# Kernel optimization log

Measured on AMD Instinct MI355X. Metric: run time of the kernel, lower is better.

## Reference

```python
import jax, jax.numpy as jnp
import numpy as np

B, H, L = 8, 256, 8192

def setup_inputs() -> dict:
    key = jax.random.key(0)
    k1, k2, k3 = jax.random.split(key, 3)
    u = jax.random.normal(k1, (B, H, L), dtype=jnp.float32)
    K = jax.random.normal(k2, (H, L), dtype=jnp.float32)
    # D ~ uniform_ring with min=max=1.0, field='real' -> random signs on unit ring
    D = jnp.where(jax.random.uniform(k3, (H,)) < 0.5, -1.0, 1.0).astype(jnp.float32)
    return {"u": u, "K": K, "D": D}

def reference(u, K, D):
    # FFT-based circular long convolution per channel: y = ifft(fft(u) * fft(K)).real
    u_s = jnp.fft.fft(u, axis=-1)            # (B,H,L) complex
    k_s = jnp.fft.fft(K, axis=-1)            # (H,L)   complex
    y = jnp.fft.ifft(u_s * k_s[None], axis=-1).real  # (B,H,L)
    y = y + D[None, :, None] * u             # skip connection D*u
    y = jnp.tanh(y)
    return y
```

## Files before the change

kernel.cpp:

```cpp
#include <hip/hip_runtime.h>
#include <math.h>


#define LL 8192
#define NT 512
#define HH 256
#define TWO_PI 6.2831853071795864f
#define CP8  0.92387953251129f
#define SP8  0.38268343236509f
#define CP4  0.70710678118654752f
#define SP4  0.70710678118654752f

__device__ __forceinline__ int SW(int e) {
    return e ^ ((e >> 3) & 0x18) ^ ((e >> 6) & 7);
}
__device__ __forceinline__ float fast_tanh(float x) {
    float e = __expf(2.0f * x);
    return 1.0f - 2.0f / (e + 1.0f);
}

template<int JT>
__device__ __forceinline__ void fill_pyr_cs(float c0, float s0, float Er, float Ei,
                                            float* twr, float* twi) {
    const int off = (1 << JT) - 1;
    twr[off] = c0; twi[off] = s0;
    #pragma unroll
    for (int m = 1; m < (1 << JT); ++m) {
        const float pr = twr[off + m - 1], pi = twi[off + m - 1];
        twr[off + m] = pr * Er - pi * Ei;
        twi[off + m] = pr * Ei + pi * Er;
    }
    #pragma unroll
    for (int j = JT - 1; j >= 0; --j) {
        #pragma unroll
        for (int m = 0; m < (1 << j); ++m) {
            const float a = twr[(2 << j) - 1 + m], b = twi[(2 << j) - 1 + m];
            twr[(1 << j) - 1 + m] = a * a - b * b;
            twi[(1 << j) - 1 + m] = 2.0f * a * b;
        }
    }
}
template<int JT>
__device__ __forceinline__ void fill_pyr(float ang0, float Er, float Ei,
                                         float* twr, float* twi) {
    float s, c;
    __sincosf(ang0, &s, &c);
    fill_pyr_cs<JT>(c, s, Er, Ei, twr, twi);
}

template<int R2>
__device__ __forceinline__ void dif_apply(float* xr, float* xi,
                                          const float* twr, const float* twi) {
    #pragma unroll
    for (int j = R2 - 1; j >= 0; --j) {
        #pragma unroll
        for (int q = 0; q < (1 << (R2 - 1)); ++q) {
            const int mm = q & ((1 << j) - 1);
            const int m0 = ((q >> j) << (j + 1)) | mm;
            const int m1 = m0 + (1 << j);
            const float wr = twr[(1 << j) - 1 + mm], wi = twi[(1 << j) - 1 + mm];
            const float ar = xr[m0], ai = xi[m0], br = xr[m1], bi = xi[m1];
            xr[m0] = ar + br; xi[m0] = ai + bi;
            const float dr = ar - br, di = ai - bi;
            xr[m1] = dr * wr - di * wi;
            xi[m1] = dr * wi + di * wr;
        }
    }
}
template<int R2>
__device__ __forceinline__ void dit_apply(float* xr, float* xi,
                                          const float* twr, const float* twi) {
    #pragma unroll
    for (int j = 0; j < R2; ++j) {
        #pragma unroll
        for (int q = 0; q < (1 << (R2 - 1)); ++q) {
            const int mm = q & ((1 << j) - 1);
            const int m0 = ((q >> j) << (j + 1)) | mm;
            const int m1 = m0 + (1 << j);
            const float wr = twr[(1 << j) - 1 + mm], wi = twi[(1 << j) - 1 + mm];
            const float br = xr[m1] * wr - xi[m1] * wi;
            const float bi = xr[m1] * wi + xi[m1] * wr;
            const float ar = xr[m0], ai = xi[m0];
            xr[m0] = ar + br; xi[m0] = ai + bi;
            xr[m1] = ar - br; xi[m1] = ai - bi;
        }
    }
}

__device__ __forceinline__ void fwd_A(float* xr, float* xi, int tid,
                                      float* re, float* im) {
    float twr[15], twi[15];
    fill_pyr<3>(-(TWO_PI / 8192.0f) * (float)tid, CP8, -SP8, twr, twi);
    dif_apply<4>(xr, xi, twr, twi);
    #pragma unroll
    for (int m = 0; m < 16; ++m) {
        const int p = SW(tid + (m << 9));
        re[p] = xr[m]; im[p] = xi[m];
    }
}

template<bool INV>
__device__ __forceinline__ void mid_M1(float* re, float* im, int lane, int wv) {
    float twr[7], twi[7];
    const float sgn = INV ? 1.0f : -1.0f;
    fill_pyr<2>(sgn * (TWO_PI / 512.0f) * (float)lane, CP4, sgn * SP4, twr, twi);
    #pragma unroll
    for (int r = 0; r < 2; ++r) {
        const int base = (((wv << 1) | r) << 9) + lane;
        float ar[8], ai[8];
        #pragma unroll
        for (int j = 0; j < 8; ++j) {
            const int p = SW(base + (j << 6));
            ar[j] = re[p]; ai[j] = im[p];
        }
        if (INV) dit_apply<3>(ar, ai, twr, twi);
        else     dif_apply<3>(ar, ai, twr, twi);
        #pragma unroll
        for (int j = 0; j < 8; ++j) {
            const int p = SW(base + (j << 6));
            re[p] = ar[j]; im[p] = ai[j];
        }
    }
}

template<bool INV>
__device__ __forceinline__ void mid_M2(float* re, float* im, int lane, int wv) {
    float twr[7], twi[7];
    const float sgn = INV ? 1.0f : -1.0f;
    fill_pyr<2>(sgn * (TWO_PI / 64.0f) * (float)(lane & 7), CP4, sgn * SP4, twr, twi);
    const int sub = ((lane >> 3) << 6) + (lane & 7);
    #pragma unroll
    for (int r = 0; r < 2; ++r) {
        const int base = (((wv << 1) | r) << 9) + sub;
        float ar[8], ai[8];
        #pragma unroll
        for (int j = 0; j < 8; ++j) {
            const int p = SW(base + (j << 3));
            ar[j] = re[p]; ai[j] = im[p];
        }
        if (INV) dit_apply<3>(ar, ai, twr, twi);
        else     dif_apply<3>(ar, ai, twr, twi);
        #pragma unroll
        for (int j = 0; j < 8; ++j) {
            const int p = SW(base + (j << 3));
            re[p] = ar[j]; im[p] = ai[j];
        }
    }
}

__global__ __launch_bounds__(NT, 4) void kfft_kernel(const float* __restrict__ K,
                                                     const float* __restrict__ D,
                                                     float2* __restrict__ Kf) {
    __shared__ float re[LL];
    __shared__ float im[LL];
    const int h = blockIdx.x;
    const int tid = threadIdx.x;
    const float* Kr = K + (size_t)h * LL;
    float xr[16], xi[16];
    #pragma unroll
    for (int m = 0; m < 16; ++m) {
        xr[m] = Kr[tid + (m << 9)];
        xi[m] = 0.0f;
    }
    fwd_A(xr, xi, tid, re, im);
    __syncthreads();

    const int lane = tid & 63, wv = tid >> 6;
    mid_M1<false>(re, im, lane, wv);
    mid_M2<false>(re, im, lane, wv);

    {
        const float dh = D[h];
        const float invN = 1.0f / (float)LL;
        float twd_r[7], twd_i[7];
        fill_pyr_cs<2>(1.0f, 0.0f, CP4, -SP4, twd_r, twd_i);
        #pragma unroll
        for (int r = 0; r < 2; ++r) {
            const int eb = (((wv << 1) | r) << 9) + (lane << 3);
            float yr[8], yi[8];
            #pragma unroll
            for (int j = 0; j < 8; ++j) {
                const int p = SW(eb + j);
                yr[j] = re[p]; yi[j] = im[p];
            }
            dif_apply<3>(yr, yi, twd_r, twd_i);
            float4* o4 = (float4*)(Kf + (size_t)h * LL + eb);
            #pragma unroll
            for (int jj = 0; jj < 4; ++jj) {
                float4 v;
                v.x = (yr[2 * jj]     + dh) * invN; v.y = yi[2 * jj]     * invN;
                v.z = (yr[2 * jj + 1] + dh) * invN; v.w = yi[2 * jj + 1] * invN;
                o4[jj] = v;
            }
        }
    }
}

__global__ __launch_bounds__(NT, 4) void conv_kernel(const float* __restrict__ u,
                                                     const float2* __restrict__ Kf,
                                                     float* __restrict__ out) {
    __shared__ float re[LL];
    __shared__ float im[LL];
    const int tid = threadIdx.x;
    const int h = blockIdx.x & (HH - 1);
    const int pr_ = blockIdx.x >> 8;
    const size_t off0 = ((size_t)(pr_ * 2) * HH + h) * LL;
    const size_t off1 = off0 + (size_t)HH * LL;
    const float* u0 = u + off0;
    const float* u1 = u + off1;

    float xr[16], xi[16];
    #pragma unroll
    for (int m = 0; m < 16; ++m) {
        xr[m] = u0[tid + (m << 9)];
        xi[m] = u1[tid + (m << 9)];
    }
    fwd_A(xr, xi, tid, re, im);
    __syncthreads();

    const int lane = tid & 63, wv = tid >> 6;
    const float2* kf = Kf + (size_t)h * LL;

    float kwr[2][8], kwi[2][8];
    #pragma unroll
    for (int r = 0; r < 2; ++r) {
        const int eb = (((wv << 1) | r) << 9) + (lane << 3);
        const float4* kp = (const float4*)(kf + eb);
        #pragma unroll
        for (int jj = 0; jj < 4; ++jj) {
            const float4 v = kp[jj];
            kwr[r][2 * jj] = v.x;     kwi[r][2 * jj] = v.y;
            kwr[r][2 * jj + 1] = v.z; kwi[r][2 * jj + 1] = v.w;
        }
    }

    mid_M1<false>(re, im, lane, wv);
    mid_M2<false>(re, im, lane, wv);

    {
        float twd_r[7], twd_i[7], twu_r[7], twu_i[7];
        fill_pyr_cs<2>(1.0f, 0.0f, CP4, -SP4, twd_r, twd_i);
        fill_pyr_cs<2>(1.0f, 0.0f, CP4, SP4, twu_r, twu_i);
        #pragma unroll
        for (int r = 0; r < 2; ++r) {
            const int eb = (((wv << 1) | r) << 9) + (lane << 3);
            float yr[8], yi[8];
            #pragma unroll
            for (int j = 0; j < 8; ++j) {
                const int p = SW(eb + j);
                yr[j] = re[p]; yi[j] = im[p];
            }
            dif_apply<3>(yr, yi, twd_r, twd_i);
            #pragma unroll
            for (int j = 0; j < 8; ++j) {
                const float a = yr[j], b = yi[j];
                yr[j] = a * kwr[r][j] - b * kwi[r][j];
                yi[j] = a * kwi[r][j] + b * kwr[r][j];
            }
            dit_apply<3>(yr, yi, twu_r, twu_i);
            #pragma unroll
            for (int j = 0; j < 8; ++j) {
                const int p = SW(eb + j);
                re[p] = yr[j]; im[p] = yi[j];
            }
        }
    }

    mid_M2<true>(re, im, lane, wv);
    mid_M1<true>(re, im, lane, wv);
    __syncthreads();

    {
        float twr[15], twi[15];
        #pragma unroll
        for (int m = 0; m < 16; ++m) {
            const int p = SW(tid + (m << 9));
            xr[m] = re[p]; xi[m] = im[p];
        }
        fill_pyr<3>((TWO_PI / 8192.0f) * (float)tid, CP8, SP8, twr, twi);
        dit_apply<4>(xr, xi, twr, twi);
    }
    float* o0 = out + off0;
    float* o1 = out + off1;
    #pragma unroll
    for (int m = 0; m < 16; ++m) {
        const int n = tid + (m << 9);
        o0[n] = fast_tanh(xr[m]);
        o1[n] = fast_tanh(xi[m]);
    }
}

extern "C" void kernel_launch(void* const* d_in, const int* in_sizes, int n_in,
                              void* d_out, int out_size, void* d_ws, size_t ws_size,
                              hipStream_t stream) {
    const float* u = (const float*)d_in[0];
    const float* K = (const float*)d_in[1];
    const float* D = (const float*)d_in[2];
    float* out = (float*)d_out;
    float2* Kf = (float2*)d_ws;

    kfft_kernel<<<dim3(HH), dim3(NT), 0, stream>>>(K, D, Kf);
    conv_kernel<<<dim3(4 * HH), dim3(NT), 0, stream>>>(u, Kf, out);
}
```

Before: 150.5 us.

## Restructure FFT to 1024 threads with 8-point radix stages and shuffle final butterfly

```diff
diff --git a/kernel.cpp b/kernel.cpp
--- a/kernel.cpp
+++ b/kernel.cpp
@@ -3,7 +3,7 @@
 
 
 #define LL 8192
-#define NT 512
+#define NT 1024
 #define HH 256
 #define TWO_PI 6.2831853071795864f
 #define CP8  0.92387953251129f
@@ -12,7 +12,7 @@
 #define SP4  0.70710678118654752f
 
 __device__ __forceinline__ int SW(int e) {
-    return e ^ ((e >> 3) & 0x18) ^ ((e >> 6) & 7);
+    return e ^ ((e >> 3) & 0x10) ^ ((e >> 5) & 0x0E);
 }
 __device__ __forceinline__ float fast_tanh(float x) {
     float e = __expf(2.0f * x);
@@ -86,69 +86,92 @@
         }
     }
 }
+template<int R2>
+__device__ __forceinline__ void dit_apply_c(float* xr, float* xi,
+                                            const float* twr, const float* twi) {
+    #pragma unroll
+    for (int j = 0; j < R2; ++j) {
+        #pragma unroll
+        for (int q = 0; q < (1 << (R2 - 1)); ++q) {
+            const int mm = q & ((1 << j) - 1);
+            const int m0 = ((q >> j) << (j + 1)) | mm;
+            const int m1 = m0 + (1 << j);
+            const float wr = twr[(1 << j) - 1 + mm], wi = -twi[(1 << j) - 1 + mm];
+            const float br = xr[m1] * wr - xi[m1] * wi;
+            const float bi = xr[m1] * wi + xi[m1] * wr;
+            const float ar = xr[m0], ai = xi[m0];
+            xr[m0] = ar + br; xi[m0] = ai + bi;
+            xr[m1] = ar - br; xi[m1] = ai - bi;
+        }
+    }
+}
+
+__device__ __forceinline__ void bfly1_shfl(float* yr, float* yi, float s) {
+    #pragma unroll
+    for (int j = 0; j < 8; ++j) {
+        const float vr = __shfl_xor(yr[j], 1);
+        const float vi = __shfl_xor(yi[j], 1);
+        yr[j] = fmaf(yr[j], s, vr);
+        yi[j] = fmaf(yi[j], s, vi);
+    }
+}
 
 __device__ __forceinline__ void fwd_A(float* xr, float* xi, int tid,
                                       float* re, float* im) {
-    float twr[15], twi[15];
-    fill_pyr<3>(-(TWO_PI / 8192.0f) * (float)tid, CP8, -SP8, twr, twi);
-    dif_apply<4>(xr, xi, twr, twi);
-    #pragma unroll
-    for (int m = 0; m < 16; ++m) {
-        const int p = SW(tid + (m << 9));
+    float twr[7], twi[7];
+    fill_pyr<2>(-(TWO_PI / 8192.0f) * (float)tid, CP4, -SP4, twr, twi);
+    dif_apply<3>(xr, xi, twr, twi);
+    #pragma unroll
+    for (int m = 0; m < 8; ++m) {
+        const int p = SW(tid + (m << 10));
         re[p] = xr[m]; im[p] = xi[m];
     }
 }
 
 template<bool INV>
-__device__ __forceinline__ void mid_M1(float* re, float* im, int lane, int wv) {
+__device__ __forceinline__ void mid_M1(float* re, float* im, int t7, int cb) {
     float twr[7], twi[7];
     const float sgn = INV ? 1.0f : -1.0f;
-    fill_pyr<2>(sgn * (TWO_PI / 512.0f) * (float)lane, CP4, sgn * SP4, twr, twi);
-    #pragma unroll
-    for (int r = 0; r < 2; ++r) {
-        const int base = (((wv << 1) | r) << 9) + lane;
-        float ar[8], ai[8];
-        #pragma unroll
-        for (int j = 0; j < 8; ++j) {
-            const int p = SW(base + (j << 6));
-            ar[j] = re[p]; ai[j] = im[p];
-        }
-        if (INV) dit_apply<3>(ar, ai, twr, twi);
-        else     dif_apply<3>(ar, ai, twr, twi);
-        #pragma unroll
-        for (int j = 0; j < 8; ++j) {
-            const int p = SW(base + (j << 6));
-            re[p] = ar[j]; im[p] = ai[j];
-        }
+    fill_pyr<2>(sgn * (TWO_PI / 1024.0f) * (float)t7, CP4, sgn * SP4, twr, twi);
+    const int base = cb + t7;
+    float ar[8], ai[8];
+    #pragma unroll
+    for (int j = 0; j < 8; ++j) {
+        const int p = SW(base + (j << 7));
+        ar[j] = re[p]; ai[j] = im[p];
+    }
+    if (INV) dit_apply<3>(ar, ai, twr, twi);
+    else     dif_apply<3>(ar, ai, twr, twi);
+    #pragma unroll
+    for (int j = 0; j < 8; ++j) {
+        const int p = SW(base + (j << 7));
+        re[p] = ar[j]; im[p] = ai[j];
     }
 }
 
 template<bool INV>
-__device__ __forceinline__ void mid_M2(float* re, float* im, int lane, int wv) {
+__device__ __forceinline__ void mid_M2(float* re, float* im, int t7, int cb) {
     float twr[7], twi[7];
     const float sgn = INV ? 1.0f : -1.0f;
-    fill_pyr<2>(sgn * (TWO_PI / 64.0f) * (float)(lane & 7), CP4, sgn * SP4, twr, twi);
-    const int sub = ((lane >> 3) << 6) + (lane & 7);
-    #pragma unroll
-    for (int r = 0; r < 2; ++r) {
-        const int base = (((wv << 1) | r) << 9) + sub;
-        float ar[8], ai[8];
-        #pragma unroll
-        for (int j = 0; j < 8; ++j) {
-            const int p = SW(base + (j << 3));
-            ar[j] = re[p]; ai[j] = im[p];
-        }
-        if (INV) dit_apply<3>(ar, ai, twr, twi);
-        else     dif_apply<3>(ar, ai, twr, twi);
-        #pragma unroll
-        for (int j = 0; j < 8; ++j) {
-            const int p = SW(base + (j << 3));
-            re[p] = ar[j]; im[p] = ai[j];
-        }
-    }
-}
-
-__global__ __launch_bounds__(NT, 4) void kfft_kernel(const float* __restrict__ K,
+    const int r_ = t7 & 15;
+    fill_pyr<2>(sgn * (TWO_PI / 128.0f) * (float)r_, CP4, sgn * SP4, twr, twi);
+    const int base = cb + ((t7 >> 4) << 7) + r_;
+    float ar[8], ai[8];
+    #pragma unroll
+    for (int j = 0; j < 8; ++j) {
+        const int p = SW(base + (j << 4));
+        ar[j] = re[p]; ai[j] = im[p];
+    }
+    if (INV) dit_apply<3>(ar, ai, twr, twi);
+    else     dif_apply<3>(ar, ai, twr, twi);
+    #pragma unroll
+    for (int j = 0; j < 8; ++j) {
+        const int p = SW(base + (j << 4));
+        re[p] = ar[j]; im[p] = ai[j];
+    }
+}
+
+__global__ __launch_bounds__(NT, 8) void kfft_kernel(const float* __restrict__ K,
                                                      const float* __restrict__ D,
                                                      float2* __restrict__ Kf) {
     __shared__ float re[LL];
@@ -156,47 +179,49 @@
     const int h = blockIdx.x;
     const int tid = threadIdx.x;
     const float* Kr = K + (size_t)h * LL;
-    float xr[16], xi[16];
-    #pragma unroll
-    for (int m = 0; m < 16; ++m) {
-        xr[m] = Kr[tid + (m << 9)];
+    float xr[8], xi[8];
+    #pragma unroll
+    for (int m = 0; m < 8; ++m) {
+        xr[m] = Kr[tid + (m << 10)];
         xi[m] = 0.0f;
     }
     fwd_A(xr, xi, tid, re, im);
     __syncthreads();
 
-    const int lane = tid & 63, wv = tid >> 6;
-    mid_M1<false>(re, im, lane, wv);
-    mid_M2<false>(re, im, lane, wv);
+    const int t7 = tid & 127;
+    const int cb = (tid >> 7) << 10;
+    mid_M1<false>(re, im, t7, cb);
+    __syncthreads();
+    mid_M2<false>(re, im, t7, cb);
 
     {
+        const int g_ = t7 >> 1, par = t7 & 1;
         const float dh = D[h];
         const float invN = 1.0f / (float)LL;
-        float twd_r[7], twd_i[7];
-        fill_pyr_cs<2>(1.0f, 0.0f, CP4, -SP4, twd_r, twd_i);
-        #pragma unroll
-        for (int r = 0; r < 2; ++r) {
-            const int eb = (((wv << 1) | r) << 9) + (lane << 3);
-            float yr[8], yi[8];
-            #pragma unroll
-            for (int j = 0; j < 8; ++j) {
-                const int p = SW(eb + j);
-                yr[j] = re[p]; yi[j] = im[p];
-            }
-            dif_apply<3>(yr, yi, twd_r, twd_i);
-            float4* o4 = (float4*)(Kf + (size_t)h * LL + eb);
-            #pragma unroll
-            for (int jj = 0; jj < 4; ++jj) {
-                float4 v;
-                v.x = (yr[2 * jj]     + dh) * invN; v.y = yi[2 * jj]     * invN;
-                v.z = (yr[2 * jj + 1] + dh) * invN; v.w = yi[2 * jj + 1] * invN;
-                o4[jj] = v;
-            }
-        }
-    }
-}
-
-__global__ __launch_bounds__(NT, 4) void conv_kernel(const float* __restrict__ u,
+        float twr[7], twi[7];
+        fill_pyr_cs<2>(par ? CP8 : 1.0f, par ? -SP8 : 0.0f, CP4, -SP4, twr, twi);
+        const int base = cb + (g_ << 4) + par;
+        const float s = par ? -1.0f : 1.0f;
+        float yr[8], yi[8];
+        #pragma unroll
+        for (int j = 0; j < 8; ++j) {
+            const int p = SW(base + (j << 1));
+            yr[j] = re[p]; yi[j] = im[p];
+        }
+        dif_apply<3>(yr, yi, twr, twi);
+        bfly1_shfl(yr, yi, s);
+        float4* o4 = (float4*)(Kf + (size_t)h * LL + cb + (t7 << 3));
+        #pragma unroll
+        for (int jj = 0; jj < 4; ++jj) {
+            float4 v;
+            v.x = (yr[2 * jj]     + dh) * invN; v.y = yi[2 * jj]     * invN;
+            v.z = (yr[2 * jj + 1] + dh) * invN; v.w = yi[2 * jj + 1] * invN;
+            o4[jj] = v;
+        }
+    }
+}
+
+__global__ __launch_bounds__(NT, 8) void conv_kernel(const float* __restrict__ u,
                                                      const float2* __restrict__ Kf,
                                                      float* __restrict__ out) {
     __shared__ float re[LL];
@@ -209,82 +234,82 @@
     const float* u0 = u + off0;
     const float* u1 = u + off1;
 
-    float xr[16], xi[16];
-    #pragma unroll
-    for (int m = 0; m < 16; ++m) {
-        xr[m] = u0[tid + (m << 9)];
-        xi[m] = u1[tid + (m << 9)];
+    float xr[8], xi[8];
+    #pragma unroll
+    for (int m = 0; m < 8; ++m) {
+        xr[m] = u0[tid + (m << 10)];
+        xi[m] = u1[tid + (m << 10)];
     }
     fwd_A(xr, xi, tid, re, im);
     __syncthreads();
 
-    const int lane = tid & 63, wv = tid >> 6;
-    const float2* kf = Kf + (size_t)h * LL;
-
-    float kwr[2][8], kwi[2][8];
-    #pragma unroll
-    for (int r = 0; r < 2; ++r) {
-        const int eb = (((wv << 1) | r) << 9) + (lane << 3);
-        const float4* kp = (const float4*)(kf + eb);
+    const int t7 = tid & 127;
+    const int cb = (tid >> 7) << 10;
+
+    float kwr[8], kwi[8];
+    {
+        const float4* kp = (const float4*)(Kf + (size_t)h * LL + cb + (t7 << 3));
         #pragma unroll
         for (int jj = 0; jj < 4; ++jj) {
             const float4 v = kp[jj];
-            kwr[r][2 * jj] = v.x;     kwi[r][2 * jj] = v.y;
-            kwr[r][2 * jj + 1] = v.z; kwi[r][2 * jj + 1] = v.w;
-        }
-    }
-
-    mid_M1<false>(re, im, lane, wv);
-    mid_M2<false>(re, im, lane, wv);
+            kwr[2 * jj]     = v.x; kwi[2 * jj]     = v.y;
+            kwr[2 * jj + 1] = v.z; kwi[2 * jj + 1] = v.w;
+        }
+    }
+
+    mid_M1<false>(re, im, t7, cb);
+    __syncthreads();
+    mid_M2<false>(re, im, t7, cb);
 
     {
-        float twd_r[7], twd_i[7], twu_r[7], twu_i[7];
-        fill_pyr_cs<2>(1.0f, 0.0f, CP4, -SP4, twd_r, twd_i);
-        fill_pyr_cs<2>(1.0f, 0.0f, CP4, SP4, twu_r, twu_i);
-        #pragma unroll
-        for (int r = 0; r < 2; ++r) {
-            const int eb = (((wv << 1) | r) << 9) + (lane << 3);
-            float yr[8], yi[8];
-            #pragma unroll
-            for (int j = 0; j < 8; ++j) {
-                const int p = SW(eb + j);
-                yr[j] = re[p]; yi[j] = im[p];
-            }
-            dif_apply<3>(yr, yi, twd_r, twd_i);
-            #pragma unroll
-            for (int j = 0; j < 8; ++j) {
-                const float a = yr[j], b = yi[j];
-                yr[j] = a * kwr[r][j] - b * kwi[r][j];
-                yi[j] = a * kwi[r][j] + b * kwr[r][j];
-            }
-            dit_apply<3>(yr, yi, twu_r, twu_i);
-            #pragma unroll
-            for (int j = 0; j < 8; ++j) {
-                const int p = SW(eb + j);
-                re[p] = yr[j]; im[p] = yi[j];
-            }
-        }
-    }
-
-    mid_M2<true>(re, im, lane, wv);
-    mid_M1<true>(re, im, lane, wv);
+        const int g_ = t7 >> 1, par = t7 & 1;
+        float twr[7], twi[7];
+        fill_pyr_cs<2>(par ? CP8 : 1.0f, par ? -SP8 : 0.0f, CP4, -SP4, twr, twi);
+        const int base = cb + (g_ << 4) + par;
+        const float s = par ? -1.0f : 1.0f;
+        float yr[8], yi[8];
+        #pragma unroll
+        for (int j = 0; j < 8; ++j) {
+            const int p = SW(base + (j << 1));
+            yr[j] = re[p]; yi[j] = im[p];
+        }
+        dif_apply<3>(yr, yi, twr, twi);
+        bfly1_shfl(yr, yi, s);
+        #pragma unroll
+        for (int j = 0; j < 8; ++j) {
+            const float a = yr[j], bb = yi[j];
+            yr[j] = a * kwr[j] - bb * kwi[j];
+            yi[j] = a * kwi[j] + bb * kwr[j];
+        }
+        bfly1_shfl(yr, yi, s);
+        dit_apply_c<3>(yr, yi, twr, twi);
+        #pragma unroll
+        for (int j = 0; j < 8; ++j) {
+            const int p = SW(base + (j << 1));
+            re[p] = yr[j]; im[p] = yi[j];
+        }
+    }
+
+    mid_M2<true>(re, im, t7, cb);
+    __syncthreads();
+    mid_M1<true>(re, im, t7, cb);
     __syncthreads();
 
     {
-        float twr[15], twi[15];
-        #pragma unroll
-        for (int m = 0; m < 16; ++m) {
-            const int p = SW(tid + (m << 9));
+        float twr[7], twi[7];
+        #pragma unroll
+        for (int m = 0; m < 8; ++m) {
+            const int p = SW(tid + (m << 10));
             xr[m] = re[p]; xi[m] = im[p];
         }
-        fill_pyr<3>((TWO_PI / 8192.0f) * (float)tid, CP8, SP8, twr, twi);
-        dit_apply<4>(xr, xi, twr, twi);
+        fill_pyr<2>((TWO_PI / 8192.0f) * (float)tid, CP4, SP4, twr, twi);
+        dit_apply<3>(xr, xi, twr, twi);
     }
     float* o0 = out + off0;
     float* o1 = out + off1;
     #pragma unroll
-    for (int m = 0; m < 16; ++m) {
-        const int n = tid + (m << 9);
+    for (int m = 0; m < 8; ++m) {
+        const int n = tid + (m << 10);
         o0[n] = fast_tanh(xr[m]);
         o1[n] = fast_tanh(xi[m]);
     }
```

Measured after the change: 189.1 us. +25.6%, slower.

## Split kernel FFT into radix-4 pass plus smaller sub-FFT kernel; retune LDS swizzle

Applied to the files above, without the earlier changes.

```diff
diff --git a/kernel.cpp b/kernel.cpp
--- a/kernel.cpp
+++ b/kernel.cpp
@@ -12,7 +12,10 @@
 #define SP4  0.70710678118654752f
 
 __device__ __forceinline__ int SW(int e) {
-    return e ^ ((e >> 3) & 0x18) ^ ((e >> 6) & 7);
+    return e ^ ((e >> 3) & 0x18) ^ ((e >> 5) & 0x0E);
+}
+__device__ __forceinline__ int SW2(int e) {
+    return e ^ (((e >> 5) & 7) << 2);
 }
 __device__ __forceinline__ float fast_tanh(float x) {
     float e = __expf(2.0f * x);
@@ -87,6 +90,7 @@
     }
 }
 
+
 __device__ __forceinline__ void fwd_A(float* xr, float* xi, int tid,
                                       float* re, float* im) {
     float twr[15], twi[15];
@@ -144,54 +148,6 @@
         for (int j = 0; j < 8; ++j) {
             const int p = SW(base + (j << 3));
             re[p] = ar[j]; im[p] = ai[j];
-        }
-    }
-}
-
-__global__ __launch_bounds__(NT, 4) void kfft_kernel(const float* __restrict__ K,
-                                                     const float* __restrict__ D,
-                                                     float2* __restrict__ Kf) {
-    __shared__ float re[LL];
-    __shared__ float im[LL];
-    const int h = blockIdx.x;
-    const int tid = threadIdx.x;
-    const float* Kr = K + (size_t)h * LL;
-    float xr[16], xi[16];
-    #pragma unroll
-    for (int m = 0; m < 16; ++m) {
-        xr[m] = Kr[tid + (m << 9)];
-        xi[m] = 0.0f;
-    }
-    fwd_A(xr, xi, tid, re, im);
-    __syncthreads();
-
-    const int lane = tid & 63, wv = tid >> 6;
-    mid_M1<false>(re, im, lane, wv);
-    mid_M2<false>(re, im, lane, wv);
-
-    {
-        const float dh = D[h];
-        const float invN = 1.0f / (float)LL;
-        float twd_r[7], twd_i[7];
-        fill_pyr_cs<2>(1.0f, 0.0f, CP4, -SP4, twd_r, twd_i);
-        #pragma unroll
-        for (int r = 0; r < 2; ++r) {
-            const int eb = (((wv << 1) | r) << 9) + (lane << 3);
-            float yr[8], yi[8];
-            #pragma unroll
-            for (int j = 0; j < 8; ++j) {
-                const int p = SW(eb + j);
-                yr[j] = re[p]; yi[j] = im[p];
-            }
-            dif_apply<3>(yr, yi, twd_r, twd_i);
-            float4* o4 = (float4*)(Kf + (size_t)h * LL + eb);
-            #pragma unroll
-            for (int jj = 0; jj < 4; ++jj) {
-                float4 v;
-                v.x = (yr[2 * jj]     + dh) * invN; v.y = yi[2 * jj]     * invN;
-                v.z = (yr[2 * jj + 1] + dh) * invN; v.w = yi[2 * jj + 1] * invN;
-                o4[jj] = v;
-            }
         }
     }
 }
@@ -219,13 +175,13 @@
     __syncthreads();
 
     const int lane = tid & 63, wv = tid >> 6;
-    const float2* kf = Kf + (size_t)h * LL;
+    const int c0 = (wv << 1);
 
     float kwr[2][8], kwi[2][8];
     #pragma unroll
     for (int r = 0; r < 2; ++r) {
-        const int eb = (((wv << 1) | r) << 9) + (lane << 3);
-        const float4* kp = (const float4*)(kf + eb);
+        const int eb = ((c0 | r) << 9) + (lane << 3);
+        const float4* kp = (const float4*)(Kf + (size_t)h * LL + eb);
         #pragma unroll
         for (int jj = 0; jj < 4; ++jj) {
             const float4 v = kp[jj];
@@ -243,7 +199,7 @@
         fill_pyr_cs<2>(1.0f, 0.0f, CP4, SP4, twu_r, twu_i);
         #pragma unroll
         for (int r = 0; r < 2; ++r) {
-            const int eb = (((wv << 1) | r) << 9) + (lane << 3);
+            const int eb = ((c0 | r) << 9) + (lane << 3);
             float yr[8], yi[8];
             #pragma unroll
             for (int j = 0; j < 8; ++j) {
@@ -290,6 +246,115 @@
     }
 }
 
+__global__ __launch_bounds__(256) void kfft1_kernel(const float* __restrict__ K,
+                                                    float2* __restrict__ Kf) {
+    const int b = blockIdx.x;
+    const int h = b >> 3, seg = b & 7;
+    const int m = (seg << 8) + threadIdx.x;
+    const float* Kr = K + (size_t)h * LL;
+    const float A = Kr[m];
+    const float B = Kr[m + 2048];
+    const float C = Kr[m + 4096];
+    const float E = Kr[m + 6144];
+    float sn, cs;
+    __sincosf(-(TWO_PI / 8192.0f) * (float)m, &sn, &cs);
+    const float c2 = cs * cs - sn * sn, s2 = 2.0f * cs * sn;
+    const float c3 = cs * c2 - sn * s2, s3 = cs * s2 + sn * c2;
+    const float p = A - C, q = B - E;
+    const float sum = A + C + B + E;
+    const float dif = A + C - B - E;
+    float2* o = Kf + (size_t)h * LL;
+    o[m]        = make_float2(sum, 0.0f);
+    o[m + 2048] = make_float2(dif * c2, dif * s2);
+    o[m + 4096] = make_float2(p * cs + q * sn, p * sn - q * cs);
+    o[m + 6144] = make_float2(p * c3 - q * s3, p * s3 + q * c3);
+}
+
+__global__ __launch_bounds__(256) void kfft2_kernel(float2* __restrict__ Kf,
+                                                    const float* __restrict__ D) {
+    __shared__ float re[2048];
+    __shared__ float im[2048];
+    const int b = blockIdx.x;
+    const int h = b >> 2, cq = b & 3;
+    const int tid = threadIdx.x;
+    float2* base = Kf + (size_t)h * LL + (cq << 11);
+
+    float xr[8], xi[8];
+    #pragma unroll
+    for (int m = 0; m < 8; ++m) {
+        const float2 v = base[tid + (m << 8)];
+        xr[m] = v.x; xi[m] = v.y;
+    }
+    {
+        float twr[7], twi[7];
+        fill_pyr<2>(-(TWO_PI / 2048.0f) * (float)tid, CP4, -SP4, twr, twi);
+        dif_apply<3>(xr, xi, twr, twi);
+    }
+    #pragma unroll
+    for (int m = 0; m < 8; ++m) {
+        const int p = SW2(tid + (m << 8));
+        re[p] = xr[m]; im[p] = xi[m];
+    }
+    __syncthreads();
+
+    {
+        const int t_ = tid & 31, sub = tid >> 5;
+        float twr[7], twi[7];
+        fill_pyr<2>(-(TWO_PI / 256.0f) * (float)t_, CP4, -SP4, twr, twi);
+        const int be = (sub << 8) + t_;
+        float ar[8], ai[8];
+        #pragma unroll
+        for (int j = 0; j < 8; ++j) {
+            const int p = SW2(be + (j << 5));
+            ar[j] = re[p]; ai[j] = im[p];
+        }
+        dif_apply<3>(ar, ai, twr, twi);
+        #pragma unroll
+        for (int j = 0; j < 8; ++j) {
+            const int p = SW2(be + (j << 5));
+            re[p] = ar[j]; im[p] = ai[j];
+        }
+    }
+
+    {
+        const int blk = tid >> 2, r = tid & 3;
+        float twr[7], twi[7];
+        fill_pyr<2>(-(TWO_PI / 32.0f) * (float)r, CP4, -SP4, twr, twi);
+        const int eb = (blk << 5) + r;
+        float yr[8], yi[8];
+        #pragma unroll
+        for (int j = 0; j < 8; ++j) {
+            const int p = SW2(eb + (j << 2));
+            yr[j] = re[p]; yi[j] = im[p];
+        }
+        dif_apply<3>(yr, yi, twr, twi);
+        const float s2 = (r < 2) ? 1.0f : -1.0f;
+        #pragma unroll
+        for (int j = 0; j < 8; ++j) {
+            const float vr = __shfl_xor(yr[j], 2);
+            const float vi = __shfl_xor(yi[j], 2);
+            const float tr = fmaf(yr[j], s2, vr);
+            const float ti = fmaf(yi[j], s2, vi);
+            yr[j] = (r == 3) ? ti : tr;
+            yi[j] = (r == 3) ? -tr : ti;
+        }
+        const float s1 = (r & 1) ? -1.0f : 1.0f;
+        #pragma unroll
+        for (int j = 0; j < 8; ++j) {
+            const float vr = __shfl_xor(yr[j], 1);
+            const float vi = __shfl_xor(yi[j], 1);
+            yr[j] = fmaf(yr[j], s1, vr);
+            yi[j] = fmaf(yi[j], s1, vi);
+        }
+        const float dh = D[h];
+        const float invN = 1.0f / (float)LL;
+        #pragma unroll
+        for (int j = 0; j < 8; ++j) {
+            base[eb + (j << 2)] = make_float2((yr[j] + dh) * invN, yi[j] * invN);
+        }
+    }
+}
+
 extern "C" void kernel_launch(void* const* d_in, const int* in_sizes, int n_in,
                               void* d_out, int out_size, void* d_ws, size_t ws_size,
                               hipStream_t stream) {
@@ -299,6 +364,7 @@
     float* out = (float*)d_out;
     float2* Kf = (float2*)d_ws;
 
-    kfft_kernel<<<dim3(HH), dim3(NT), 0, stream>>>(K, D, Kf);
+    kfft1_kernel<<<dim3(8 * HH), dim3(256), 0, stream>>>(K, Kf);
+    kfft2_kernel<<<dim3(4 * HH), dim3(256), 0, stream>>>(Kf, D);
     conv_kernel<<<dim3(4 * HH), dim3(NT), 0, stream>>>(u, Kf, out);
 }
```

Measured after the change: 154.4 us. +2.6%, slower.
